# Optimization experiments

Hardware: AMD Instinct MI355X
Metric: run time of the kernel (lower is better)

The kernel has to match this reference:

```python
import jax, jax.numpy as jnp
import numpy as np

V = 50257   # vocab_size
BLOCK = 1024
D = 768     # n_embd
H = 12      # n_head
L = 2       # n_layer
B = 4
T = 1024
EPS = 1e-5


def _ln(x, g, b):
    mu = jnp.mean(x, axis=-1, keepdims=True)
    var = jnp.var(x, axis=-1, keepdims=True)
    return (x - mu) * jax.lax.rsqrt(var + EPS) * g + b


def setup_inputs() -> dict:
    key = jax.random.key(0)
    ks = jax.random.split(key, 10)
    def n(k, shape, std=0.02):
        return jax.random.normal(k, shape, jnp.float32) * std
    proj_std = (2 * L) ** -0.5  # set_scale init in the torch code
    return dict(
        idx=jax.random.randint(ks[0], (B, T), 0, V),
        layer_num=0,
        wte=n(ks[1], (V, D)),
        wpe=n(ks[2], (BLOCK, D)),
        ln1_g=jnp.ones((L, D)), ln1_b=jnp.zeros((L, D)),
        attn_w=n(ks[3], (L, D, 3 * D)), attn_b=jnp.zeros((L, 3 * D)),
        proj_w=n(ks[4], (L, D, D), proj_std), proj_b=jnp.zeros((L, D)),
        ln2_g=jnp.ones((L, D)), ln2_b=jnp.zeros((L, D)),
        fc_w=n(ks[5], (L, D, 4 * D)), fc_b=jnp.zeros((L, 4 * D)),
        fc2_w=n(ks[6], (L, 4 * D, D), proj_std), fc2_b=jnp.zeros((L, D)),
        lnf_g=jnp.ones((D,)), lnf_b=jnp.zeros((D,)),
        lm_w=n(ks[7], (D, V)),
    )


def _gpt(idx, wte, wpe, ln1_g, ln1_b, attn_w, attn_b, proj_w, proj_b,
         ln2_g, ln2_b, fc_w, fc_b, fc2_w, fc2_b, lnf_g, lnf_b, lm_w):
    b, t = idx.shape
    hd = D // H
    x = wte[idx] + wpe[:t]                      # [B,T,D]
    causal = jnp.tril(jnp.ones((t, t), bool))   # [T,T]
    for l in range(L):
        h = _ln(x, ln1_g[l], ln1_b[l])
        qkv = h @ attn_w[l] + attn_b[l]          # [B,T,3D]
        q, k, v = jnp.split(qkv, 3, axis=-1)
        q = q.reshape(b, t, H, hd)
        k = k.reshape(b, t, H, hd)
        v = v.reshape(b, t, H, hd)
        att = jnp.einsum('bqhd,bkhd->bhqk', q, k) * (1.0 / np.sqrt(hd))
        att = jnp.where(causal, att, -jnp.inf)
        att = jax.nn.softmax(att, axis=-1)
        y = jnp.einsum('bhqk,bkhd->bqhd', att, v).reshape(b, t, D)
        x = x + (y @ proj_w[l] + proj_b[l])
        h2 = _ln(x, ln2_g[l], ln2_b[l])
        h2 = jax.nn.gelu(h2 @ fc_w[l] + fc_b[l], approximate=True)  # tanh GELU
        x = x + (h2 @ fc2_w[l] + fc2_b[l])
    x = _ln(x, lnf_g, lnf_b)
    return x @ lm_w                             # [B,T,V] logits


def reference(idx, layer_num, wte, wpe, ln1_g, ln1_b, attn_w, attn_b,
              proj_w, proj_b, ln2_g, ln2_b, fc_w, fc_b, fc2_w, fc2_b,
              lnf_g, lnf_b, lm_w):
    # layer_num is unused in the forward math (pipeline-stage bookkeeping)
    return _gpt(idx, wte, wpe, ln1_g, ln1_b, attn_w, attn_b, proj_w, proj_b,
                ln2_g, ln2_b, fc_w, fc_b, fc2_w, fc2_b, lnf_g, lnf_b, lm_w)
```

## Files before the change

kernel.cpp:

```cpp
#include <hip/hip_runtime.h>
#include <hip/hip_bf16.h>
#include <cstdint>
#include <cstddef>

typedef __bf16 bf16_t;
typedef __bf16 bf16x8 __attribute__((ext_vector_type(8)));
typedef float f32x4 __attribute__((ext_vector_type(4)));

#define GLB_AS(p) ((__attribute__((address_space(1))) void*)(void*)(p))
#define LDS_AS(p) ((__attribute__((address_space(3))) void*)(p))

__device__ __forceinline__ float wave_red_sum(float v) {
#pragma unroll
  for (int o = 1; o < 64; o <<= 1) v += __shfl_xor(v, o, 64);
  return v;
}

__device__ __forceinline__ float gelu_tanh(float v) {
  float c = 0.7978845608028654f * (v + 0.044715f * v * v * v);
  return 0.5f * v * (1.0f + tanhf(c));
}

__device__ __forceinline__ f32x4 mfma16(f32x4 a, f32x4 b, f32x4 c) {
  return __builtin_amdgcn_mfma_f32_16x16x32_bf16(
      __builtin_bit_cast(bf16x8, a), __builtin_bit_cast(bf16x8, b), c, 0, 0, 0);
}

__device__ __forceinline__ int swz(int off) { return off ^ ((off >> 3) & 0x70); }

#define PHASE_WAIT()                                    \
  asm volatile("s_waitcnt lgkmcnt(0)" ::: "memory");    \
  __builtin_amdgcn_sched_barrier(0)

__global__ __launch_bounds__(256) void embed_ln_k(const int* __restrict__ idx,
                                                  const float* __restrict__ wte,
                                                  const float* __restrict__ wpe,
                                                  const float* __restrict__ g,
                                                  const float* __restrict__ b,
                                                  float* __restrict__ x,
                                                  bf16_t* __restrict__ out) {
  const int m = blockIdx.x;
  const int tid = threadIdx.x;
  const int tok = idx[m];
  const int t = m & 1023;
  float v[3];
#pragma unroll
  for (int i = 0; i < 3; ++i) {
    const int d = tid + i * 256;
    v[i] = wte[(size_t)tok * 768 + d] + wpe[(size_t)t * 768 + d];
    x[(size_t)m * 768 + d] = v[i];
  }
  float s = v[0] + v[1] + v[2];
  float q = v[0] * v[0] + v[1] * v[1] + v[2] * v[2];
  s = wave_red_sum(s);
  q = wave_red_sum(q);
  __shared__ float sm[8];
  const int wave = tid >> 6, lane = tid & 63;
  if (lane == 0) { sm[wave] = s; sm[4 + wave] = q; }
  __syncthreads();
  s = sm[0] + sm[1] + sm[2] + sm[3];
  q = sm[4] + sm[5] + sm[6] + sm[7];
  const float mu = s * (1.0f / 768.0f);
  const float var = q * (1.0f / 768.0f) - mu * mu;
  const float rs = rsqrtf(var + 1e-5f);
  bf16_t* orow = out + (size_t)m * 768;
#pragma unroll
  for (int i = 0; i < 3; ++i) {
    const int d = tid + i * 256;
    orow[d] = (bf16_t)((v[i] - mu) * rs * g[d] + b[d]);
  }
}

__global__ __launch_bounds__(256) void ln_k(const float* __restrict__ x,
                                            const float* __restrict__ g,
                                            const float* __restrict__ b,
                                            bf16_t* __restrict__ out) {
  const int row = blockIdx.x;
  const int tid = threadIdx.x;
  const float* xr = x + (size_t)row * 768;
  float v0 = xr[tid], v1 = xr[tid + 256], v2 = xr[tid + 512];
  float s = v0 + v1 + v2;
  float q = v0 * v0 + v1 * v1 + v2 * v2;
  s = wave_red_sum(s);
  q = wave_red_sum(q);
  __shared__ float sm[8];
  const int wave = tid >> 6, lane = tid & 63;
  if (lane == 0) { sm[wave] = s; sm[4 + wave] = q; }
  __syncthreads();
  s = sm[0] + sm[1] + sm[2] + sm[3];
  q = sm[4] + sm[5] + sm[6] + sm[7];
  const float mu = s * (1.0f / 768.0f);
  const float var = q * (1.0f / 768.0f) - mu * mu;
  const float rs = rsqrtf(var + 1e-5f);
  bf16_t* orow = out + (size_t)row * 768;
#pragma unroll
  for (int i = 0; i < 3; ++i) {
    const int d = tid + i * 256;
    const float v = (i == 0 ? v0 : (i == 1 ? v1 : v2));
    orow[d] = (bf16_t)((v - mu) * rs * g[d] + b[d]);
  }
}

struct TJob { const float* W; bf16_t* WT; int K, N, Npad, blk0, nbx; };
struct TJobs { TJob j[9]; };

__global__ __launch_bounds__(256) void transp_all(TJobs jobs) {
  __shared__ float tile[32][33];
  const int bidx = blockIdx.x;
  int ji = 0;
#pragma unroll
  for (int u = 1; u < 9; ++u)
    if (bidx >= jobs.j[u].blk0) ji = u;
  const TJob jb = jobs.j[ji];
  const int lb = bidx - jb.blk0;
  const int n0 = (lb % jb.nbx) * 32, k0 = (lb / jb.nbx) * 32;
  const int tx = threadIdx.x, ty = threadIdx.y;
#pragma unroll
  for (int i = 0; i < 4; ++i) {
    const int k = k0 + ty + i * 8, n = n0 + tx;
    tile[ty + i * 8][tx] = (k < jb.K && n < jb.N) ? jb.W[(size_t)k * jb.N + n] : 0.0f;
  }
  __syncthreads();
#pragma unroll
  for (int i = 0; i < 4; ++i) {
    const int n = n0 + ty + i * 8, k = k0 + tx;
    if (n < jb.Npad && k < jb.K) jb.WT[(size_t)n * jb.K + k] = (bf16_t)tile[tx][ty + i * 8];
  }
}

__global__ __launch_bounds__(256) void vtr_k(const bf16_t* __restrict__ qkv,
                                             bf16_t* __restrict__ vt) {
  __shared__ bf16_t tile[64][72];
  const int bh = blockIdx.y;
  const int h = bh % 12, b = bh / 12;
  const int t0 = blockIdx.x * 64;
  const int tx = threadIdx.x & 63;
  const int wv = threadIdx.x >> 6;
#pragma unroll
  for (int i = 0; i < 16; ++i) {
    const int r = wv * 16 + i;
    tile[r][tx] = qkv[(size_t)(b * 1024 + t0 + r) * 2304 + 1536 + h * 64 + tx];
  }
  __syncthreads();
#pragma unroll
  for (int i = 0; i < 16; ++i) {
    const int d = wv * 16 + i;
    vt[((size_t)bh * 64 + d) * 1024 + t0 + tx] = tile[tx][d];
  }
}

template <int EPI>
__global__ __launch_bounds__(512, 2) void gemm256p(const bf16_t* __restrict__ A,
                                                   const bf16_t* __restrict__ BT,
                                                   const float* __restrict__ bias,
                                                   void* __restrict__ outp,
                                                   int M, int N, int K, int Nout,
                                                   int ntiles) {
  __shared__ __align__(16) char lds[131072];
  const int tid = threadIdx.x;
  const int lane = tid & 63, wave = tid >> 6;
  const int wr = wave >> 2, wc = wave & 3;
  const int fr = lane & 15, fq = lane >> 4;

  const int nmblk = M >> 8;
  const int G = gridDim.x;
  const int flat = blockIdx.x;
  const int xcd = flat & 7, rest = flat >> 3;
  const int q8 = G >> 3, r8 = G & 7;
  const int bid = (xcd < r8 ? xcd * (q8 + 1) : r8 * (q8 + 1) + (xcd - r8) * q8) + rest;
  const int qt = ntiles / G, rt = ntiles % G;
  const int tstart = bid * qt + (bid < rt ? bid : rt);
  const int cnt = qt + (bid < rt ? 1 : 0);
  if (cnt == 0) return;
  const int NT = K >> 6;
  const int sEnd = (tstart + cnt) * NT;

  int srow[4], scb[4];
#pragma unroll
  for (int u = 0; u < 4; ++u) {
    const int s = swz(u * 8192 + tid * 16);
    srow[u] = s >> 7;
    scb[u] = s & 127;
  }
  const char* Abase = (const char*)A;
  const char* Bbase = (const char*)BT;

  auto stageA = [&](int pi, int u, int m0x, int tauK) {
    const char* src = Abase + ((size_t)(m0x + srow[u]) * K + tauK * 64) * 2 + scb[u];
    __builtin_amdgcn_global_load_lds(GLB_AS(src),
        LDS_AS(&lds[pi * 32768 + u * 8192 + wave * 1024]), 16, 0, 0);
  };
  auto stageB = [&](int pi, int u, int n0x, int tauK) {
    const char* src = Bbase + ((size_t)(n0x + srow[u]) * K + tauK * 64) * 2 + scb[u];
    __builtin_amdgcn_global_load_lds(GLB_AS(src),
        LDS_AS(&lds[65536 + pi * 32768 + u * 8192 + wave * 1024]), 16, 0, 0);
  };
  auto rdA = [&](int pi, int msub, int i, int kk) -> f32x4 {
    const int row = wr * 128 + msub * 64 + i * 16 + fr;
    const int off = swz(row * 128 + kk * 64 + fq * 16);
    return *(const f32x4*)(&lds[pi * 32768 + off]);
  };
  auto rdB = [&](int pi, int j, int kk) -> f32x4 {
    const int row = wc * 64 + j * 16 + fr;
    const int off = swz(row * 128 + kk * 64 + fq * 16);
    return *(const f32x4*)(&lds[65536 + pi * 32768 + off]);
  };

  int m0 = (tstart % nmblk) << 8, n0 = (tstart / nmblk) << 8;
  int m1 = m0, n1 = n0, t1 = 1;
  int m2 = m0, n2 = n0, t2 = 2;
  auto adv = [&](int& mx, int& nx, int& tx) {
    if (++tx == NT) { tx = 0; mx += 256; if (mx >= M) { mx = 0; nx += 256; } }
  };

  f32x4 acc[8][4] = {};
  f32x4 a_[4][2], b_[4][2];

  stageA(0, 0, m0, 0); stageA(0, 1, m0, 0); stageA(0, 2, m0, 0); stageA(0, 3, m0, 0);
  stageB(0, 0, n0, 0); stageB(0, 1, n0, 0); stageB(0, 2, n0, 0); stageB(0, 3, n0, 0);
  stageA(1, 0, m1, t1); stageA(1, 2, m1, t1); stageB(1, 0, n1, t1); stageB(1, 1, n1, t1);
  stageA(1, 1, m1, t1); stageA(1, 3, m1, t1);
  asm volatile("s_waitcnt vmcnt(6)" ::: "memory");
  __builtin_amdgcn_s_barrier();

  int pi = 0;
  int s = tstart * NT;
  for (int t = 0; t < cnt; ++t) {
    for (int tau = 0; tau < NT; ++tau, ++s) {
      const bool h1 = (s + 1 < sEnd), h2 = (s + 2 < sEnd);
#pragma unroll
      for (int i = 0; i < 4; ++i) { a_[i][0] = rdA(pi, 0, i, 0); a_[i][1] = rdA(pi, 0, i, 1); }
#pragma unroll
      for (int j = 0; j < 2; ++j) { b_[j][0] = rdB(pi, j, 0); b_[j][1] = rdB(pi, j, 1); }
      if (h1) { stageB(pi ^ 1, 2, n1, t1); stageB(pi ^ 1, 3, n1, t1); }
      __builtin_amdgcn_s_barrier();
      PHASE_WAIT();
      __builtin_amdgcn_s_setprio(1);
#pragma unroll
      for (int i = 0; i < 4; ++i)
#pragma unroll
        for (int j = 0; j < 2; ++j) {
          acc[i][j] = mfma16(a_[i][0], b_[j][0], acc[i][j]);
          acc[i][j] = mfma16(a_[i][1], b_[j][1], acc[i][j]);
        }
      __builtin_amdgcn_s_setprio(0);
      __builtin_amdgcn_s_barrier();
#pragma unroll
      for (int j = 0; j < 2; ++j) { b_[2 + j][0] = rdB(pi, 2 + j, 0); b_[2 + j][1] = rdB(pi, 2 + j, 1); }
      if (h2) { stageA(pi, 0, m2, t2); stageA(pi, 2, m2, t2); }
      __builtin_amdgcn_s_barrier();
      PHASE_WAIT();
      __builtin_amdgcn_s_setprio(1);
#pragma unroll
      for (int i = 0; i < 4; ++i)
#pragma unroll
        for (int j = 0; j < 2; ++j) {
          acc[i][2 + j] = mfma16(a_[i][0], b_[2 + j][0], acc[i][2 + j]);
          acc[i][2 + j] = mfma16(a_[i][1], b_[2 + j][1], acc[i][2 + j]);
        }
      __builtin_amdgcn_s_setprio(0);
      __builtin_amdgcn_s_barrier();
#pragma unroll
      for (int i = 0; i < 4; ++i) { a_[i][0] = rdA(pi, 1, i, 0); a_[i][1] = rdA(pi, 1, i, 1); }
      if (h2) { stageB(pi, 0, n2, t2); stageB(pi, 1, n2, t2); }
      __builtin_amdgcn_s_barrier();
      PHASE_WAIT();
      __builtin_amdgcn_s_setprio(1);
#pragma unroll
      for (int i = 0; i < 4; ++i)
#pragma unroll
        for (int j = 0; j < 2; ++j) {
          acc[4 + i][j] = mfma16(a_[i][0], b_[j][0], acc[4 + i][j]);
          acc[4 + i][j] = mfma16(a_[i][1], b_[j][1], acc[4 + i][j]);
        }
      __builtin_amdgcn_s_setprio(0);
      __builtin_amdgcn_s_barrier();
      if (h2) {
        stageA(pi, 1, m2, t2); stageA(pi, 3, m2, t2);
        asm volatile("s_waitcnt vmcnt(6)" ::: "memory");
      } else {
        asm volatile("s_waitcnt vmcnt(0)" ::: "memory");
      }
      __builtin_amdgcn_s_barrier();
      __builtin_amdgcn_sched_barrier(0);
      __builtin_amdgcn_s_setprio(1);
#pragma unroll
      for (int i = 0; i < 4; ++i)
#pragma unroll
        for (int j = 0; j < 2; ++j) {
          acc[4 + i][2 + j] = mfma16(a_[i][0], b_[2 + j][0], acc[4 + i][2 + j]);
          acc[4 + i][2 + j] = mfma16(a_[i][1], b_[2 + j][1], acc[4 + i][2 + j]);
        }
      __builtin_amdgcn_s_setprio(0);
      __builtin_amdgcn_s_barrier();
      pi ^= 1;
      adv(m1, n1, t1);
      adv(m2, n2, t2);
    }

#pragma unroll
    for (int i8 = 0; i8 < 8; ++i8) {
#pragma unroll
      for (int j4 = 0; j4 < 4; ++j4) {
        const int r0 = m0 + wr * 128 + i8 * 16 + fq * 4;
        const int c = n0 + wc * 64 + j4 * 16 + fr;
        float bv = 0.0f;
        if constexpr (EPI != 3) bv = bias[c];
#pragma unroll
        for (int e = 0; e < 4; ++e) {
          const int r = r0 + e;
          float v = acc[i8][j4][e] + bv;
          if constexpr (EPI == 0) {
            ((bf16_t*)outp)[(size_t)r * N + c] = (bf16_t)v;
          } else if constexpr (EPI == 1) {
            ((bf16_t*)outp)[(size_t)r * N + c] = (bf16_t)gelu_tanh(v);
          } else {
            if (c < Nout) ((float*)outp)[(size_t)r * Nout + c] = v;
          }
        }
      }
    }
#pragma unroll
    for (int i8 = 0; i8 < 8; ++i8)
#pragma unroll
      for (int j4 = 0; j4 < 4; ++j4) acc[i8][j4] = (f32x4){0.0f, 0.0f, 0.0f, 0.0f};
    m0 += 256; if (m0 >= M) { m0 = 0; n0 += 256; }
  }
}

template <int EPI>
__global__ __launch_bounds__(256) void gemm_bt(const bf16_t* __restrict__ A,
                                               const bf16_t* __restrict__ BT,
                                               const float* __restrict__ bias,
                                               void* __restrict__ outp,
                                               float* __restrict__ resid,
                                               int M, int N, int K, int Nout) {
  __shared__ __align__(16) bf16_t As[128 * 32];
  __shared__ __align__(16) bf16_t Bs[128 * 32];
  const int tid = threadIdx.x;
  const int lane = tid & 63, wave = tid >> 6;

  const int nmblk = M >> 7;
  const int nwg = gridDim.x;
  const int flat = blockIdx.x;
  const int xcd = flat & 7, rest = flat >> 3;
  const int q8 = nwg >> 3, r8 = nwg & 7;
  const int wgid = (xcd < r8 ? xcd * (q8 + 1) : r8 * (q8 + 1) + (xcd - r8) * q8) + rest;
  const int m0 = (wgid % nmblk) * 128;
  const int n0 = (wgid / nmblk) * 128;

  const int wr = wave >> 1, wc = wave & 1;
  const int fr = lane & 15, fq = lane >> 4;
  const int se = tid * 8;
  const int srow = se >> 5, scol = se & 31;
  const int wvbase = wave * 512;
  f32x4 acc[4][4] = {};

  for (int k0 = 0; k0 < K; k0 += 32) {
#pragma unroll
    for (int r = 0; r < 2; ++r) {
      __builtin_amdgcn_global_load_lds(
          GLB_AS(&A[(size_t)(m0 + srow + r * 64) * K + k0 + scol]),
          LDS_AS(&As[wvbase + r * 2048]), 16, 0, 0);
      __builtin_amdgcn_global_load_lds(
          GLB_AS(&BT[(size_t)(n0 + srow + r * 64) * K + k0 + scol]),
          LDS_AS(&Bs[wvbase + r * 2048]), 16, 0, 0);
    }
    __syncthreads();
    bf16x8 a[4], b[4];
#pragma unroll
    for (int i = 0; i < 4; ++i) {
      a[i] = *(const bf16x8*)(&As[(wr * 64 + i * 16 + fr) * 32 + fq * 8]);
      b[i] = *(const bf16x8*)(&Bs[(wc * 64 + i * 16 + fr) * 32 + fq * 8]);
    }
#pragma unroll
    for (int i = 0; i < 4; ++i)
#pragma unroll
      for (int j = 0; j < 4; ++j)
        acc[i][j] = __builtin_amdgcn_mfma_f32_16x16x32_bf16(a[i], b[j], acc[i][j], 0, 0, 0);
    __syncthreads();
  }

#pragma unroll
  for (int i = 0; i < 4; ++i) {
#pragma unroll
    for (int j = 0; j < 4; ++j) {
      const int r0 = m0 + wr * 64 + i * 16 + fq * 4;
      const int c = n0 + wc * 64 + j * 16 + fr;
      const float bv = bias[c];
#pragma unroll
      for (int e = 0; e < 4; ++e) {
        const int r = r0 + e;
        resid[(size_t)r * N + c] += acc[i][j][e] + bv;
      }
    }
  }
}

__global__ __launch_bounds__(256) void fattn_k(const bf16_t* __restrict__ qkv,
                                               const bf16_t* __restrict__ vt,
                                               bf16_t* __restrict__ y) {
  __shared__ bf16_t Pl[4][16][40];
  const int wave = threadIdx.x >> 6, lane = threadIdx.x & 63;
  const int wid = blockIdx.x * 4 + wave;
  const int qt = wid & 63;
  const int bh = wid >> 6;
  const int h = bh % 12, b = bh / 12;
  const int fr = lane & 15, fq = lane >> 4;

  const bf16_t* qrow = qkv + (size_t)(b * 1024 + qt * 16 + fr) * 2304 + h * 64;
  const bf16x8 qf0 = *(const bf16x8*)(qrow + fq * 8);
  const bf16x8 qf1 = *(const bf16x8*)(qrow + 32 + fq * 8);

  const bf16_t* kbase = qkv + (size_t)b * 1024 * 2304 + 768 + h * 64 + fq * 8;
  const bf16_t* vbase = vt + ((size_t)bh * 64 + fr) * 1024 + fq * 8;

  f32x4 o[4] = {};
  float mrun[4], lrun[4];
#pragma unroll
  for (int e = 0; e < 4; ++e) { mrun[e] = -1e30f; lrun[e] = 0.0f; }

  const int qg = qt * 16 + fq * 4;
  const int kv_end = qt * 16 + 16;

  for (int kv0 = 0; kv0 < kv_end; kv0 += 32) {
    f32x4 s0 = {}, s1 = {};
    {
      const bf16_t* k0p = kbase + (size_t)(kv0 + fr) * 2304;
      const bf16_t* k1p = kbase + (size_t)(kv0 + 16 + fr) * 2304;
      const bf16x8 kf00 = *(const bf16x8*)(k0p);
      const bf16x8 kf01 = *(const bf16x8*)(k0p + 32);
      const bf16x8 kf10 = *(const bf16x8*)(k1p);
      const bf16x8 kf11 = *(const bf16x8*)(k1p + 32);
      s0 = __builtin_amdgcn_mfma_f32_16x16x32_bf16(qf0, kf00, s0, 0, 0, 0);
      s0 = __builtin_amdgcn_mfma_f32_16x16x32_bf16(qf1, kf01, s0, 0, 0, 0);
      s1 = __builtin_amdgcn_mfma_f32_16x16x32_bf16(qf0, kf10, s1, 0, 0, 0);
      s1 = __builtin_amdgcn_mfma_f32_16x16x32_bf16(qf1, kf11, s1, 0, 0, 0);
    }
    float v0[4], v1[4];
#pragma unroll
    for (int e = 0; e < 4; ++e) {
      v0[e] = (kv0 + fr <= qg + e) ? s0[e] * 0.125f : -1e30f;
      v1[e] = (kv0 + 16 + fr <= qg + e) ? s1[e] * 0.125f : -1e30f;
    }
    float p0[4], p1[4];
#pragma unroll
    for (int e = 0; e < 4; ++e) {
      float mx = fmaxf(v0[e], v1[e]);
      mx = fmaxf(mx, __shfl_xor(mx, 1, 64));
      mx = fmaxf(mx, __shfl_xor(mx, 2, 64));
      mx = fmaxf(mx, __shfl_xor(mx, 4, 64));
      mx = fmaxf(mx, __shfl_xor(mx, 8, 64));
      const float mnew = fmaxf(mrun[e], mx);
      p0[e] = __expf(v0[e] - mnew);
      p1[e] = __expf(v1[e] - mnew);
      float rs = p0[e] + p1[e];
      rs += __shfl_xor(rs, 1, 64);
      rs += __shfl_xor(rs, 2, 64);
      rs += __shfl_xor(rs, 4, 64);
      rs += __shfl_xor(rs, 8, 64);
      const float alpha = __expf(mrun[e] - mnew);
      lrun[e] = lrun[e] * alpha + rs;
      mrun[e] = mnew;
#pragma unroll
      for (int db = 0; db < 4; ++db) o[db][e] *= alpha;
    }
#pragma unroll
    for (int e = 0; e < 4; ++e) {
      Pl[wave][fq * 4 + e][fr] = (bf16_t)p0[e];
      Pl[wave][fq * 4 + e][16 + fr] = (bf16_t)p1[e];
    }
    asm volatile("s_waitcnt lgkmcnt(0)" ::: "memory");
    const bf16x8 pf = *(const bf16x8*)(&Pl[wave][fr][fq * 8]);
#pragma unroll
    for (int db = 0; db < 4; ++db) {
      const bf16x8 vf = *(const bf16x8*)(vbase + (size_t)db * 16 * 1024 + kv0);
      o[db] = __builtin_amdgcn_mfma_f32_16x16x32_bf16(pf, vf, o[db], 0, 0, 0);
    }
  }

#pragma unroll
  for (int db = 0; db < 4; ++db) {
#pragma unroll
    for (int e = 0; e < 4; ++e) {
      const int q = qt * 16 + fq * 4 + e;
      const int d = db * 16 + fr;
      y[(size_t)(b * 1024 + q) * 768 + h * 64 + d] = (bf16_t)(o[db][e] / lrun[e]);
    }
  }
}

extern "C" void kernel_launch(void* const* d_in, const int* in_sizes, int n_in,
                              void* d_out, int out_size, void* d_ws, size_t ws_size,
                              hipStream_t stream) {
  constexpr int Bb = 4, T = 1024, Lg = 2, Vr = 50257, Vp = 50432;
  constexpr int M = Bb * T;

  const int* idx = (const int*)d_in[0];
  const float* wte = (const float*)d_in[2];
  const float* wpe = (const float*)d_in[3];
  const float* ln1_g = (const float*)d_in[4];
  const float* ln1_b = (const float*)d_in[5];
  const float* attn_w = (const float*)d_in[6];
  const float* attn_b = (const float*)d_in[7];
  const float* proj_w = (const float*)d_in[8];
  const float* proj_b = (const float*)d_in[9];
  const float* ln2_g = (const float*)d_in[10];
  const float* ln2_b = (const float*)d_in[11];
  const float* fc_w = (const float*)d_in[12];
  const float* fc_b = (const float*)d_in[13];
  const float* fc2_w = (const float*)d_in[14];
  const float* fc2_b = (const float*)d_in[15];
  const float* lnf_g = (const float*)d_in[16];
  const float* lnf_b = (const float*)d_in[17];
  const float* lm_w = (const float*)d_in[18];
  float* out = (float*)d_out;

  char* wp = (char*)d_ws;
  auto take = [&](size_t n) { char* p = wp; wp += (n + 255) & ~(size_t)255; return p; };
  bf16_t* WqkvT = (bf16_t*)take((size_t)Lg * 2304 * 768 * 2);
  bf16_t* WprojT = (bf16_t*)take((size_t)Lg * 768 * 768 * 2);
  bf16_t* WfcT = (bf16_t*)take((size_t)Lg * 3072 * 768 * 2);
  bf16_t* Wfc2T = (bf16_t*)take((size_t)Lg * 768 * 3072 * 2);
  bf16_t* WlmT = (bf16_t*)take((size_t)Vp * 768 * 2);
  float* xb = (float*)take((size_t)M * 768 * 4);
  bf16_t* hb = (bf16_t*)take((size_t)M * 768 * 2);
  bf16_t* qkvb = (bf16_t*)take((size_t)M * 2304 * 2);
  bf16_t* yb = (bf16_t*)take((size_t)M * 768 * 2);
  bf16_t* actb = (bf16_t*)take((size_t)M * 3072 * 2);
  bf16_t* vtb = (bf16_t*)take((size_t)M * 768 * 2);

  TJobs jobs;
  int blk = 0, ji = 0;
  auto addjob = [&](const float* W, bf16_t* WT, int K, int N, int Npad) {
    const int nbx = Npad / 32, nby = K / 32;
    jobs.j[ji++] = TJob{W, WT, K, N, Npad, blk, nbx};
    blk += nbx * nby;
  };
  for (int l = 0; l < Lg; ++l) {
    addjob(attn_w + (size_t)l * 768 * 2304, WqkvT + (size_t)l * 2304 * 768, 768, 2304, 2304);
    addjob(proj_w + (size_t)l * 768 * 768, WprojT + (size_t)l * 768 * 768, 768, 768, 768);
    addjob(fc_w + (size_t)l * 768 * 3072, WfcT + (size_t)l * 3072 * 768, 768, 3072, 3072);
    addjob(fc2_w + (size_t)l * 3072 * 768, Wfc2T + (size_t)l * 768 * 3072, 3072, 768, 768);
  }
  addjob(lm_w, WlmT, 768, Vr, Vp);
  transp_all<<<blk, dim3(32, 8), 0, stream>>>(jobs);

  embed_ln_k<<<M, 256, 0, stream>>>(idx, wte, wpe, ln1_g, ln1_b, xb, hb);

  for (int l = 0; l < Lg; ++l) {
    if (l > 0) ln_k<<<M, 256, 0, stream>>>(xb, ln1_g + l * 768, ln1_b + l * 768, hb);
    gemm256p<0><<<(M / 256) * (2304 / 256), 512, 0, stream>>>(
        hb, WqkvT + (size_t)l * 2304 * 768, attn_b + l * 2304, qkvb,
        M, 2304, 768, 2304, (M / 256) * (2304 / 256));
    vtr_k<<<dim3(T / 64, Bb * 12), 256, 0, stream>>>(qkvb, vtb);
    fattn_k<<<(Bb * 12 * 64) / 4, 256, 0, stream>>>(qkvb, vtb, yb);
    gemm_bt<2><<<(M / 128) * (768 / 128), 256, 0, stream>>>(
        yb, WprojT + (size_t)l * 768 * 768, proj_b + l * 768, nullptr, xb,
        M, 768, 768, 768);
    ln_k<<<M, 256, 0, stream>>>(xb, ln2_g + l * 768, ln2_b + l * 768, hb);
    gemm256p<1><<<(M / 256) * (3072 / 256), 512, 0, stream>>>(
        hb, WfcT + (size_t)l * 3072 * 768, fc_b + l * 3072, actb,
        M, 3072, 768, 3072, (M / 256) * (3072 / 256));
    gemm_bt<2><<<(M / 128) * (768 / 128), 256, 0, stream>>>(
        actb, Wfc2T + (size_t)l * 768 * 3072, fc2_b + l * 768, nullptr, xb,
        M, 768, 3072, 768);
  }
  ln_k<<<M, 256, 0, stream>>>(xb, lnf_g, lnf_b, hb);
  gemm256p<3><<<512, 512, 0, stream>>>(
      hb, WlmT, nullptr, out, M, Vp, 768, Vr, (M / 256) * (Vp / 256));
}
```

Measured before the change: 1.209 ms.

## Double-buffer the 128-tile residual GEMM with swizzled LDS and async prefetch

Replaces the single-buffered residual-add GEMM used for the attention projection and FC2 with a double-buffered version. The next K-tile's global-to-LDS loads are issued before the current tile's MFMAs finish, using vmcnt waits and raw barriers instead of two __syncthreads per step. LDS rows are XOR-swizzled to reduce bank conflicts on the fragment reads, and MFMA sections get raised wave priority. The cost is twice the LDS per block and more delicate waitcnt and barrier ordering.

Result: faster. 1.140 ms (-5.7%).

```diff
diff --git a/kernel.cpp b/kernel.cpp
--- a/kernel.cpp
+++ b/kernel.cpp
@@ -27,6 +27,7 @@
 }
 
 __device__ __forceinline__ int swz(int off) { return off ^ ((off >> 3) & 0x70); }
+__device__ __forceinline__ int swz64(int off) { return off ^ ((off >> 3) & 0x30); }
 
 #define PHASE_WAIT()                                    \
   asm volatile("s_waitcnt lgkmcnt(0)" ::: "memory");    \
@@ -328,17 +329,16 @@
   }
 }
 
-template <int EPI>
-__global__ __launch_bounds__(256) void gemm_bt(const bf16_t* __restrict__ A,
-                                               const bf16_t* __restrict__ BT,
-                                               const float* __restrict__ bias,
-                                               void* __restrict__ outp,
-                                               float* __restrict__ resid,
-                                               int M, int N, int K, int Nout) {
-  __shared__ __align__(16) bf16_t As[128 * 32];
-  __shared__ __align__(16) bf16_t Bs[128 * 32];
+__global__ __launch_bounds__(256) void gemm128p(const bf16_t* __restrict__ A,
+                                                const bf16_t* __restrict__ BT,
+                                                const float* __restrict__ bias,
+                                                float* __restrict__ resid,
+                                                int M, int N, int K) {
+  __shared__ __align__(16) char lds[32768];
   const int tid = threadIdx.x;
   const int lane = tid & 63, wave = tid >> 6;
+  const int wr = wave >> 1, wc = wave & 1;
+  const int fr = lane & 15, fq = lane >> 4;
 
   const int nmblk = M >> 7;
   const int nwg = gridDim.x;
@@ -348,37 +348,66 @@
   const int wgid = (xcd < r8 ? xcd * (q8 + 1) : r8 * (q8 + 1) + (xcd - r8) * q8) + rest;
   const int m0 = (wgid % nmblk) * 128;
   const int n0 = (wgid / nmblk) * 128;
-
-  const int wr = wave >> 1, wc = wave & 1;
-  const int fr = lane & 15, fq = lane >> 4;
-  const int se = tid * 8;
-  const int srow = se >> 5, scol = se & 31;
-  const int wvbase = wave * 512;
+  const int NT = K >> 5;
+
+  int srow[2], scb[2];
+#pragma unroll
+  for (int u = 0; u < 2; ++u) {
+    const int s = swz64(u * 4096 + tid * 16);
+    srow[u] = s >> 6;
+    scb[u] = s & 63;
+  }
+  const char* Abase = (const char*)A;
+  const char* Bbase = (const char*)BT;
+
+  auto stage = [&](int pi, int tauK) {
+#pragma unroll
+    for (int u = 0; u < 2; ++u) {
+      const char* srcA = Abase + ((size_t)(m0 + srow[u]) * K + tauK * 32) * 2 + scb[u];
+      __builtin_amdgcn_global_load_lds(GLB_AS(srcA),
+          LDS_AS(&lds[pi * 8192 + u * 4096 + wave * 1024]), 16, 0, 0);
+      const char* srcB = Bbase + ((size_t)(n0 + srow[u]) * K + tauK * 32) * 2 + scb[u];
+      __builtin_amdgcn_global_load_lds(GLB_AS(srcB),
+          LDS_AS(&lds[16384 + pi * 8192 + u * 4096 + wave * 1024]), 16, 0, 0);
+    }
+  };
+  auto rdA = [&](int pi, int i) -> f32x4 {
+    const int off = swz64((wr * 64 + i * 16 + fr) * 64 + fq * 16);
+    return *(const f32x4*)(&lds[pi * 8192 + off]);
+  };
+  auto rdB = [&](int pi, int j) -> f32x4 {
+    const int off = swz64((wc * 64 + j * 16 + fr) * 64 + fq * 16);
+    return *(const f32x4*)(&lds[16384 + pi * 8192 + off]);
+  };
+
   f32x4 acc[4][4] = {};
 
-  for (int k0 = 0; k0 < K; k0 += 32) {
-#pragma unroll
-    for (int r = 0; r < 2; ++r) {
-      __builtin_amdgcn_global_load_lds(
-          GLB_AS(&A[(size_t)(m0 + srow + r * 64) * K + k0 + scol]),
-          LDS_AS(&As[wvbase + r * 2048]), 16, 0, 0);
-      __builtin_amdgcn_global_load_lds(
-          GLB_AS(&BT[(size_t)(n0 + srow + r * 64) * K + k0 + scol]),
-          LDS_AS(&Bs[wvbase + r * 2048]), 16, 0, 0);
-    }
-    __syncthreads();
-    bf16x8 a[4], b[4];
-#pragma unroll
-    for (int i = 0; i < 4; ++i) {
-      a[i] = *(const bf16x8*)(&As[(wr * 64 + i * 16 + fr) * 32 + fq * 8]);
-      b[i] = *(const bf16x8*)(&Bs[(wc * 64 + i * 16 + fr) * 32 + fq * 8]);
-    }
+  stage(0, 0); stage(1, 1);
+  asm volatile("s_waitcnt vmcnt(4)" ::: "memory");
+  __builtin_amdgcn_s_barrier();
+
+  for (int s = 0; s < NT; ++s) {
+    const int pi = s & 1;
+    f32x4 a_[4], b_[4];
+#pragma unroll
+    for (int i = 0; i < 4; ++i) a_[i] = rdA(pi, i);
+#pragma unroll
+    for (int j = 0; j < 4; ++j) b_[j] = rdB(pi, j);
+    PHASE_WAIT();
+    __builtin_amdgcn_s_setprio(1);
 #pragma unroll
     for (int i = 0; i < 4; ++i)
 #pragma unroll
-      for (int j = 0; j < 4; ++j)
-        acc[i][j] = __builtin_amdgcn_mfma_f32_16x16x32_bf16(a[i], b[j], acc[i][j], 0, 0, 0);
-    __syncthreads();
+      for (int j = 0; j < 4; ++j) acc[i][j] = mfma16(a_[i], b_[j], acc[i][j]);
+    __builtin_amdgcn_s_setprio(0);
+    __builtin_amdgcn_s_barrier();
+    if (s + 2 < NT) {
+      stage(pi, s + 2);
+      asm volatile("s_waitcnt vmcnt(4)" ::: "memory");
+    } else {
+      asm volatile("s_waitcnt vmcnt(0)" ::: "memory");
+    }
+    __builtin_amdgcn_s_barrier();
   }
 
 #pragma unroll
@@ -555,16 +584,14 @@
         M, 2304, 768, 2304, (M / 256) * (2304 / 256));
     vtr_k<<<dim3(T / 64, Bb * 12), 256, 0, stream>>>(qkvb, vtb);
     fattn_k<<<(Bb * 12 * 64) / 4, 256, 0, stream>>>(qkvb, vtb, yb);
-    gemm_bt<2><<<(M / 128) * (768 / 128), 256, 0, stream>>>(
-        yb, WprojT + (size_t)l * 768 * 768, proj_b + l * 768, nullptr, xb,
-        M, 768, 768, 768);
+    gemm128p<<<(M / 128) * (768 / 128), 256, 0, stream>>>(
+        yb, WprojT + (size_t)l * 768 * 768, proj_b + l * 768, xb, M, 768, 768);
     ln_k<<<M, 256, 0, stream>>>(xb, ln2_g + l * 768, ln2_b + l * 768, hb);
     gemm256p<1><<<(M / 256) * (3072 / 256), 512, 0, stream>>>(
         hb, WfcT + (size_t)l * 3072 * 768, fc_b + l * 3072, actb,
         M, 3072, 768, 3072, (M / 256) * (3072 / 256));
-    gemm_bt<2><<<(M / 128) * (768 / 128), 256, 0, stream>>>(
-        actb, Wfc2T + (size_t)l * 768 * 3072, fc2_b + l * 768, nullptr, xb,
-        M, 768, 3072, 768);
+    gemm128p<<<(M / 128) * (768 / 128), 256, 0, stream>>>(
+        actb, Wfc2T + (size_t)l * 768 * 3072, fc2_b + l * 768, xb, M, 768, 3072);
   }
   ln_k<<<M, 256, 0, stream>>>(xb, lnf_g, lnf_b, hb);
   gemm256p<3><<<512, 512, 0, stream>>>(
```
